# Kernel tuning notes

Measured on AMD Instinct MI355X. Metric: run time of the kernel, lower is better.

## Reference

```python
import jax, jax.numpy as jnp
import numpy as np

B, N, DIN, DOUT, EIN, EOUT = 8, 256, 64, 64, 64, 64


def setup_inputs() -> dict:
    key = jax.random.key(0)
    ks = jax.random.split(key, 9)
    A = jax.random.randint(ks[0], (B, N, N), 0, 2).astype(jnp.float32)  # {0,1} connectivity
    emb_node = jax.random.normal(ks[1], (B, N, DIN), dtype=jnp.float32)
    emb_edge = jax.random.normal(ks[2], (B, N, N, EIN), dtype=jnp.float32)
    s_n = 1.0 / np.sqrt(DIN)
    s_e = 1.0 / np.sqrt(EIN)
    Wn = jax.random.uniform(ks[3], (DIN, DOUT), minval=-s_n, maxval=s_n)
    bn = jax.random.uniform(ks[4], (DOUT,), minval=-s_n, maxval=s_n)
    Wsn = jax.random.uniform(ks[5], (DIN, DOUT), minval=-s_n, maxval=s_n)
    bsn = jax.random.uniform(ks[6], (DOUT,), minval=-s_n, maxval=s_n)
    We = jax.random.uniform(ks[7], (EIN, EOUT), minval=-s_e, maxval=s_e)
    be = jax.random.uniform(ks[8], (EOUT,), minval=-s_e, maxval=s_e)
    return {"A": A, "emb_node": emb_node, "emb_edge": emb_edge,
            "Wn": Wn, "bn": bn, "Wsn": Wsn, "bsn": bsn, "We": We, "be": be}


def reference(A, emb_node, emb_edge, Wn, bn, Wsn, bsn, We, be):
    # mode=1 (default) of ChannelIndependentConv
    node_x = emb_node @ Wn + bn          # [B,N,DOUT]
    node_sx = emb_node @ Wsn + bsn       # [B,N,DOUT]
    edge_x = emb_edge @ We + be          # [B,N,N,EOUT]
    # mask edges by connectivity, then channel-independent aggregation:
    # out[b,i,c] = sum_j A[b,i,j] * edge_x[b,i,j,c] * node_x[b,j,c]
    Ae = A[..., None] * edge_x           # [B,N,N,EOUT]
    agg = jnp.einsum('bijc,bjc->bic', Ae, node_x)  # [B,N,DOUT]
    node_out = jax.nn.relu(agg) + jax.nn.relu(node_sx)
    edge_out = jax.nn.relu(edge_x)
    return node_out, edge_out
```

## Files before the change

kernel.cpp:

```cpp
#include <hip/hip_runtime.h>
#include <hip/hip_bf16.h>

#define BN   2048
#define NN   256
#define CH   64

__global__ __launch_bounds__(256) void node_kernel(
    const float* __restrict__ emb_node, const float* __restrict__ Wn,
    const float* __restrict__ bn, const float* __restrict__ Wsn,
    const float* __restrict__ bsn, float* __restrict__ node_x,
    float* __restrict__ rsx) {
  __shared__ float s_emb[4][CH];
  const int r = threadIdx.x >> 6;
  const int c = threadIdx.x & 63;
  const int row = blockIdx.x * 4 + r;
  s_emb[r][c] = emb_node[row * CH + c];
  __syncthreads();
  float a1 = bn[c], a2 = bsn[c];
#pragma unroll
  for (int k = 0; k < CH; ++k) {
    const float e = s_emb[r][k];
    a1 = fmaf(e, Wn[k * CH + c], a1);
    a2 = fmaf(e, Wsn[k * CH + c], a2);
  }
  node_x[row * CH + c] = a1;
  rsx[row * CH + c] = fmaxf(a2, 0.0f);
}

__global__ __launch_bounds__(256) void edge_kernel(
    const float* __restrict__ A, const float* __restrict__ emb_edge,
    const float* __restrict__ We, const float* __restrict__ be,
    const float* __restrict__ node_x, const float* __restrict__ rsx,
    float* __restrict__ node_out, float* __restrict__ edge_out) {
  const int bi  = blockIdx.x;
  const int b   = bi >> 8;
  const int tid = threadIdx.x;
  const int c   = tid & 63;
  const int jj  = tid >> 6;

  float w[CH];
#pragma unroll
  for (int k = 0; k < CH; ++k) w[k] = We[k * CH + c];
  const float bias = be[c];

  __shared__ float s_emb[16][CH];
  __shared__ float s_A[NN];
  __shared__ float s_agg[CH];

  s_A[tid] = A[(size_t)bi * NN + tid];
  if (tid < CH) s_agg[tid] = 0.0f;

  const float* __restrict__ erow = emb_edge + (size_t)bi * NN * CH;
  float* __restrict__ eout       = edge_out + (size_t)bi * NN * CH;
  const float* __restrict__ nx   = node_x + (size_t)b * NN * CH;

  float agg = 0.0f;
  __syncthreads();

  for (int j0 = 0; j0 < NN; j0 += 16) {
    __syncthreads();
    const float4 v = *(const float4*)(erow + j0 * CH + tid * 4);
    *(float4*)(&s_emb[0][0] + tid * 4) = v;
    __syncthreads();
#pragma unroll
    for (int t = 0; t < 4; ++t) {
      const int jl = jj + 4 * t;
      const int j  = j0 + jl;
      float acc = bias;
#pragma unroll
      for (int k = 0; k < CH; ++k)
        acc = fmaf(s_emb[jl][k], w[k], acc);
      eout[j * CH + c] = fmaxf(acc, 0.0f);
      agg = fmaf(s_A[j] * acc, nx[j * CH + c], agg);
    }
  }
  atomicAdd(&s_agg[c], agg);
  __syncthreads();
  if (tid < CH) {
    node_out[(size_t)bi * CH + tid] =
        fmaxf(s_agg[tid], 0.0f) + rsx[(size_t)bi * CH + tid];
  }
}

extern "C" void kernel_launch(void* const* d_in, const int* in_sizes, int n_in,
                              void* d_out, int out_size, void* d_ws, size_t ws_size,
                              hipStream_t stream) {
  const float* A        = (const float*)d_in[0];
  const float* emb_node = (const float*)d_in[1];
  const float* emb_edge = (const float*)d_in[2];
  const float* Wn       = (const float*)d_in[3];
  const float* bn       = (const float*)d_in[4];
  const float* Wsn      = (const float*)d_in[5];
  const float* bsn      = (const float*)d_in[6];
  const float* We       = (const float*)d_in[7];
  const float* be       = (const float*)d_in[8];

  float* node_out = (float*)d_out;
  float* edge_out = (float*)d_out + (size_t)BN * CH;

  float* node_x = (float*)d_ws;
  float* rsx    = (float*)d_ws + (size_t)BN * CH;

  hipLaunchKernelGGL(node_kernel, dim3(BN / 4), dim3(256), 0, stream,
                     emb_node, Wn, bn, Wsn, bsn, node_x, rsx);
  hipLaunchKernelGGL(edge_kernel, dim3(BN), dim3(256), 0, stream,
                     A, emb_edge, We, be, node_x, rsx, node_out, edge_out);
}
```

Before: 295.5 us.

## Compute edge projection with bf16 MFMA and drop shared-memory staging

Replaces the scalar FMA edge projection with 16x16x32 bf16 MFMA instructions, converting emb_edge and We to bf16 in registers. Each wave handles 16 output channels and loads edge rows directly from global memory instead of staging them through shared memory with barriers. The per-channel aggregation now reduces with cross-lane shuffles instead of a shared atomic add. This trades fp32 accuracy of edge_x for bf16 inputs, which may affect tolerance.

Result: slower. 335.2 us (+13.5%).

```diff
diff --git a/kernel.cpp b/kernel.cpp
--- a/kernel.cpp
+++ b/kernel.cpp
@@ -4,6 +4,15 @@
 #define BN   2048
 #define NN   256
 #define CH   64
+
+typedef __attribute__((ext_vector_type(8))) short short8;
+typedef __attribute__((ext_vector_type(4))) float fv4;
+
+static __device__ inline short f2bf(float f) {
+  unsigned u = __float_as_uint(f);
+  u += 0x7FFF + ((u >> 16) & 1);
+  return (short)(u >> 16);
+}
 
 __global__ __launch_bounds__(256) void node_kernel(
     const float* __restrict__ emb_node, const float* __restrict__ Wn,
@@ -27,58 +36,64 @@
   rsx[row * CH + c] = fmaxf(a2, 0.0f);
 }
 
-__global__ __launch_bounds__(256) void edge_kernel(
+__global__ __launch_bounds__(256) void edge_mfma_kernel(
     const float* __restrict__ A, const float* __restrict__ emb_edge,
     const float* __restrict__ We, const float* __restrict__ be,
     const float* __restrict__ node_x, const float* __restrict__ rsx,
     float* __restrict__ node_out, float* __restrict__ edge_out) {
-  const int bi  = blockIdx.x;
-  const int b   = bi >> 8;
-  const int tid = threadIdx.x;
-  const int c   = tid & 63;
-  const int jj  = tid >> 6;
+  const int bi   = blockIdx.x;
+  const int b    = bi >> 8;
+  const int lane = threadIdx.x & 63;
+  const int wave = threadIdx.x >> 6;
+  const int l15  = lane & 15;
+  const int quad = lane >> 4;
+  const int c    = wave * 16 + l15;
 
-  float w[CH];
+  short8 bfrag[2];
 #pragma unroll
-  for (int k = 0; k < CH; ++k) w[k] = We[k * CH + c];
+  for (int h = 0; h < 2; ++h)
+#pragma unroll
+    for (int j = 0; j < 8; ++j)
+      bfrag[h][j] = f2bf(We[(h * 32 + quad * 8 + j) * CH + c]);
   const float bias = be[c];
 
-  __shared__ float s_emb[16][CH];
-  __shared__ float s_A[NN];
-  __shared__ float s_agg[CH];
-
-  s_A[tid] = A[(size_t)bi * NN + tid];
-  if (tid < CH) s_agg[tid] = 0.0f;
-
-  const float* __restrict__ erow = emb_edge + (size_t)bi * NN * CH;
-  float* __restrict__ eout       = edge_out + (size_t)bi * NN * CH;
+  const float* __restrict__ ee   = emb_edge + (size_t)bi * NN * CH;
+  float*       __restrict__ eo   = edge_out + (size_t)bi * NN * CH;
+  const float* __restrict__ Arow = A + (size_t)bi * NN;
   const float* __restrict__ nx   = node_x + (size_t)b * NN * CH;
 
   float agg = 0.0f;
-  __syncthreads();
 
-  for (int j0 = 0; j0 < NN; j0 += 16) {
-    __syncthreads();
-    const float4 v = *(const float4*)(erow + j0 * CH + tid * 4);
-    *(float4*)(&s_emb[0][0] + tid * 4) = v;
-    __syncthreads();
+#pragma unroll 4
+  for (int jt = 0; jt < 16; ++jt) {
+    const int j0 = jt * 16;
+    fv4 acc = {0.0f, 0.0f, 0.0f, 0.0f};
 #pragma unroll
-    for (int t = 0; t < 4; ++t) {
-      const int jl = jj + 4 * t;
-      const int j  = j0 + jl;
-      float acc = bias;
+    for (int h = 0; h < 2; ++h) {
+      const float* p = ee + (size_t)(j0 + l15) * CH + h * 32 + quad * 8;
+      const fv4 v0 = *(const fv4*)p;
+      const fv4 v1 = *(const fv4*)(p + 4);
+      short8 af;
+      af[0] = f2bf(v0[0]); af[1] = f2bf(v0[1]);
+      af[2] = f2bf(v0[2]); af[3] = f2bf(v0[3]);
+      af[4] = f2bf(v1[0]); af[5] = f2bf(v1[1]);
+      af[6] = f2bf(v1[2]); af[7] = f2bf(v1[3]);
+      acc = __builtin_amdgcn_mfma_f32_16x16x32_bf16(af, bfrag[h], acc, 0, 0, 0);
+    }
 #pragma unroll
-      for (int k = 0; k < CH; ++k)
-        acc = fmaf(s_emb[jl][k], w[k], acc);
-      eout[j * CH + c] = fmaxf(acc, 0.0f);
-      agg = fmaf(s_A[j] * acc, nx[j * CH + c], agg);
+    for (int r = 0; r < 4; ++r) {
+      const int row = j0 + quad * 4 + r;
+      const float ex = acc[r] + bias;
+      eo[row * CH + c] = fmaxf(ex, 0.0f);
+      agg = fmaf(Arow[row] * ex, nx[row * CH + c], agg);
     }
   }
-  atomicAdd(&s_agg[c], agg);
-  __syncthreads();
-  if (tid < CH) {
-    node_out[(size_t)bi * CH + tid] =
-        fmaxf(s_agg[tid], 0.0f) + rsx[(size_t)bi * CH + tid];
+
+  agg += __shfl_xor(agg, 16, 64);
+  agg += __shfl_xor(agg, 32, 64);
+  if (quad == 0) {
+    node_out[(size_t)bi * CH + c] =
+        fmaxf(agg, 0.0f) + rsx[(size_t)bi * CH + c];
   }
 }
 
@@ -103,6 +118,6 @@
 
   hipLaunchKernelGGL(node_kernel, dim3(BN / 4), dim3(256), 0, stream,
                      emb_node, Wn, bn, Wsn, bsn, node_x, rsx);
-  hipLaunchKernelGGL(edge_kernel, dim3(BN), dim3(256), 0, stream,
+  hipLaunchKernelGGL(edge_mfma_kernel, dim3(BN), dim3(256), 0, stream,
                      A, emb_edge, We, be, node_x, rsx, node_out, edge_out);
 }
```
